# Kernel optimization log

Hardware: AMD Instinct MI355X
Metric: run time of the kernel (lower is better)

## Reference

```python
import jax, jax.numpy as jnp
import numpy as np

N0, N1, N2, N3, B = 120000, 20000, 6000, 1600, 64
E1, E2, E3 = 480000, 144000, 38400
KS = 5  # kernel size per dim; K = 125 total


def spline_basis(pseudo, ks=KS):
    # open B-spline basis, degree 1, over [0,1]^3 (torch_spline_conv semantics)
    p = pseudo * (ks - 1)                       # (E,3)
    lo = jnp.clip(jnp.floor(p), 0.0, ks - 2.0)  # (E,3)
    f = p - lo                                  # fractional part
    bits = jnp.array([[(s >> d) & 1 for d in range(3)] for s in range(8)],
                     dtype=jnp.float32)         # (8,3) corner offsets
    w = jnp.where(bits[None] > 0, f[:, None, :], 1.0 - f[:, None, :])  # (E,8,3)
    basis = w[..., 0] * w[..., 1] * w[..., 2]   # (E,8)
    strides = jnp.array([1.0, ks, ks * ks], dtype=jnp.float32)
    kidx = ((lo[:, None, :] + bits[None]) * strides).sum(-1).astype(jnp.int32)  # (E,8)
    return basis, kidx


def spline_conv(x, edge_index, pseudo, W, root, bias, num_nodes):
    src, dst = edge_index[0], edge_index[1]
    basis, kidx = spline_basis(pseudo)                   # (E,8), (E,8)
    XW = jnp.einsum('ni,kio->nko', x, W)                 # (N,K,out)
    taps = XW[src[:, None], kidx]                        # (E,8,out) gather
    msg = (taps * basis[..., None]).sum(axis=1)          # (E,out)
    agg = jax.ops.segment_sum(msg, dst, num_segments=num_nodes)
    deg = jax.ops.segment_sum(jnp.ones_like(dst, jnp.float32), dst,
                              num_segments=num_nodes)
    agg = agg / jnp.maximum(deg, 1.0)[:, None]           # mean aggregation
    return agg + x @ root + bias


def seg_max(x, seg, n):
    v = jax.ops.segment_max(x, seg, num_segments=n)
    return jnp.where(jnp.isfinite(v), v, 0.0)  # empty voxels -> 0


def setup_inputs() -> dict:
    key = jax.random.key(0)
    ks = jax.random.split(key, 24)
    return {
        'x0': jax.random.uniform(ks[0], (N0, 1), jnp.float32),
        'cluster0': jax.random.randint(ks[1], (N0,), 0, N1),
        'edge1': jax.random.randint(ks[2], (2, E1), 0, N1),
        'pseudo1': jax.random.uniform(ks[3], (E1, 3), jnp.float32),
        'W1': jax.random.normal(ks[4], (125, 1, 64), jnp.float32) * 0.1,
        'root1': jax.random.normal(ks[5], (1, 64), jnp.float32) * 0.1,
        'b1': jnp.zeros((64,), jnp.float32),
        'cluster1': jax.random.randint(ks[6], (N1,), 0, N2),
        'edge2': jax.random.randint(ks[7], (2, E2), 0, N2),
        'pseudo2': jax.random.uniform(ks[8], (E2, 3), jnp.float32),
        'W2': jax.random.normal(ks[9], (125, 64, 64), jnp.float32) * 0.05,
        'root2': jax.random.normal(ks[10], (64, 64), jnp.float32) * 0.05,
        'b2': jnp.zeros((64,), jnp.float32),
        'cluster2': jax.random.randint(ks[11], (N2,), 0, N3),
        'edge3': jax.random.randint(ks[12], (2, E3), 0, N3),
        'pseudo3': jax.random.uniform(ks[13], (E3, 3), jnp.float32),
        'W3': jax.random.normal(ks[14], (125, 64, 128), jnp.float32) * 0.05,
        'root3': jax.random.normal(ks[15], (64, 128), jnp.float32) * 0.05,
        'b3': jnp.zeros((128,), jnp.float32),
        'cluster3': jax.random.randint(ks[16], (N3,), 0, B * 8),
        'fc1_w': jax.random.normal(ks[17], (1024, 256), jnp.float32) * 0.03,
        'fc1_b': jnp.zeros((256,), jnp.float32),
        'fc2_w': jax.random.normal(ks[18], (256, 10), jnp.float32) * 0.06,
        'fc2_b': jnp.zeros((10,), jnp.float32),
    }


def reference(x0, cluster0, edge1, pseudo1, W1, root1, b1,
              cluster1, edge2, pseudo2, W2, root2, b2,
              cluster2, edge3, pseudo3, W3, root3, b3,
              cluster3, fc1_w, fc1_b, fc2_w, fc2_b):
    x = seg_max(x0, cluster0, N1)                       # sparse voxel max pool 1
    x = jax.nn.elu(spline_conv(x, edge1, pseudo1, W1, root1, b1, N1))
    x = seg_max(x, cluster1, N2)                        # pool 2
    x = jax.nn.elu(spline_conv(x, edge2, pseudo2, W2, root2, b2, N2))
    x = seg_max(x, cluster2, N3)                        # pool 3
    x = jax.nn.elu(spline_conv(x, edge3, pseudo3, W3, root3, b3, N3))
    x = seg_max(x, cluster3, B * 8)                     # dense 2x2x2 voxel pool
    x = x.reshape(B, 8 * 128)
    x = jax.nn.elu(x @ fc1_w + fc1_b)
    x = x @ fc2_w + fc2_b
    return jax.nn.log_softmax(x, axis=1)
```

## Files before the change

kernel.cpp:

```cpp
#include <hip/hip_runtime.h>
#include <hip/hip_bf16.h>
#include <hip/hip_fp16.h>
#include <math.h>

#define N0c 120000
#define N1c 20000
#define N2c 6000
#define N3c 1600
#define E1c 480000
#define E2c 144000
#define E3c 38400

#define HB1 256
#define HB2 480
#define HB3 160
#define WCVB 125
#define WC1B 32
#define SS0B  469
#define OFFB  345
#define DECB  79

typedef __attribute__((ext_vector_type(8))) short short8;
typedef __attribute__((ext_vector_type(8))) _Float16 half8;
typedef __attribute__((ext_vector_type(4))) float f32x4;

__device__ __forceinline__ float eluf(float x) {
    return x > 0.0f ? x : expm1f(x);
}

__device__ __forceinline__ unsigned f2sort(float f) {
    unsigned u = __float_as_uint(f);
    return (u & 0x80000000u) ? ~u : (u | 0x80000000u);
}
__device__ __forceinline__ float sort2f(unsigned u) {
    unsigned bits = (u & 0x80000000u) ? (u & 0x7FFFFFFFu) : ~u;
    return __uint_as_float(bits);
}
__device__ __forceinline__ unsigned short f2bf(float v) {
    unsigned u = __float_as_uint(v);
    unsigned r = (u + 0x7FFFu + ((u >> 16) & 1u)) >> 16;
    return (unsigned short)r;
}
__device__ __forceinline__ unsigned short f2h(float v) {
    return __half_as_ushort(__float2half(v));
}
__device__ __forceinline__ float h2f(unsigned short u) {
    return __half2float(__ushort_as_half(u));
}

__global__ __launch_bounds__(256) void hist_all(
    const int* __restrict__ edge1, const int* __restrict__ edge2,
    const int* __restrict__ edge3,
    const float* __restrict__ pseudo2, const float* __restrict__ pseudo3,
    const float* __restrict__ W2, const float* __restrict__ W3,
    const float* __restrict__ W1,
    const float* __restrict__ x0, const int* __restrict__ cluster0,
    int* __restrict__ blockCnt1, int* __restrict__ binTot1,
    int* __restrict__ blockCnt2, int* __restrict__ binTot2, int* __restrict__ cntD2,
    int* __restrict__ blockCnt3, int* __restrict__ binTot3, int* __restrict__ cntD3,
    unsigned short* __restrict__ W2t, unsigned short* __restrict__ W3t,
    unsigned short* __restrict__ W1t,
    unsigned* __restrict__ xm1)
{
    __shared__ float smf[64 * 129];
    int* h = (int*)smf;
    int b = blockIdx.x, t = threadIdx.x;
    if (b < HB1) {
        for (int i = t; i < 1250; i += 256) h[i] = 0;
        __syncthreads();
        for (int e = b * 256 + t; e < E1c; e += HB1 * 256)
            atomicAdd(&h[edge1[E1c + e] >> 4], 1);
        __syncthreads();
        for (int i = t; i < 1250; i += 256) {
            int v = h[i];
            blockCnt1[i * HB1 + b] = v;
            if (v) atomicAdd(&binTot1[i], v);
        }
    } else if (b < HB1 + HB2 + HB3) {
        bool is2 = b < HB1 + HB2;
        int rb = is2 ? (b - HB1) : (b - HB1 - HB2);
        int nblk = is2 ? HB2 : HB3;
        int E = is2 ? E2c : E3c;
        const int* edge = is2 ? edge2 : edge3;
        const float* pseudo = is2 ? pseudo2 : pseudo3;
        int* blockCnt = is2 ? blockCnt2 : blockCnt3;
        int* binTot = is2 ? binTot2 : binTot3;
        int* dstCnt = is2 ? cntD2 : cntD3;
        int nb = is2 ? HB2 : HB3;
        if (t < 64) h[t] = 0;
        __syncthreads();
        for (int e = rb * 256 + t; e < E; e += nblk * 256) {
            int c = 0, mul = 1;
            #pragma unroll
            for (int d = 0; d < 3; d++) {
                float p = pseudo[e * 3 + d] * 4.0f;
                float l = fminf(fmaxf(floorf(p), 0.0f), 3.0f);
                c += (int)l * mul;
                mul <<= 2;
            }
            atomicAdd(&h[c], 1);
            atomicAdd(&dstCnt[edge[E + e]], 1);
        }
        __syncthreads();
        if (t < 64) {
            int v = h[t];
            blockCnt[t * nb + rb] = v;
            if (v) atomicAdd(&binTot[t], v);
        }
    } else if (b < HB1 + HB2 + HB3 + WCVB) {
        int k = b - (HB1 + HB2 + HB3);
        for (int idx = t; idx < 4096; idx += 256) {
            int n = idx & 63, ic = idx >> 6;
            smf[ic * 65 + n] = W2[((size_t)k * 64 + ic) * 64 + n];
        }
        __syncthreads();
        for (int idx = t; idx < 4096; idx += 256) {
            int ic = idx & 63, n = idx >> 6;
            int f = ic >> 5, q = (ic >> 3) & 3, hh = ic & 7;
            int cb = n >> 4, mc = n & 15;
            W2t[((size_t)((k * 2 + f) * 4 + cb)) * 512 + mc * 32 + q * 8 + hh]
                = f2bf(smf[ic * 65 + n]);
        }
    } else if (b < HB1 + HB2 + HB3 + 2 * WCVB) {
        int k = b - (HB1 + HB2 + HB3 + WCVB);
        for (int idx = t; idx < 8192; idx += 256) {
            int n = idx & 127, ic = idx >> 7;
            smf[ic * 129 + n] = W3[((size_t)k * 64 + ic) * 128 + n];
        }
        __syncthreads();
        for (int idx = t; idx < 8192; idx += 256) {
            int ic = idx & 63, n = idx >> 6;
            int f = ic >> 5, q = (ic >> 3) & 3, hh = ic & 7;
            int cb = n >> 4, mc = n & 15;
            W3t[((size_t)((k * 2 + f) * 8 + cb)) * 512 + mc * 32 + q * 8 + hh]
                = f2bf(smf[ic * 129 + n]);
        }
    } else if (b < HB1 + HB2 + HB3 + 2 * WCVB + WC1B) {
        int idx = (b - (HB1 + HB2 + HB3 + 2 * WCVB)) * 256 + t;
        int n = idx >> 7, k = idx & 127;
        W1t[idx] = (k < 125) ? f2h(W1[k * 64 + n]) : (unsigned short)0;
    } else {
        int idx = (b - (HB1 + HB2 + HB3 + 2 * WCVB + WC1B)) * 256 + t;
        if (idx < N0c)
            atomicMax(&xm1[cluster0[idx]], f2sort(x0[idx]));
    }
}

__global__ __launch_bounds__(256) void plan_tot(
    const int* __restrict__ binTot1, int* __restrict__ start1,
    const int* __restrict__ binTot2, int* __restrict__ binCnt2,
    int* __restrict__ binStart2, int* __restrict__ blkPrefix2,
    int* __restrict__ chunkBin2, int* __restrict__ chunkOff2,
    const int* __restrict__ binTot3, int* __restrict__ binCnt3,
    int* __restrict__ binStart3, int* __restrict__ blkPrefix3,
    int* __restrict__ chunkBin3, int* __restrict__ chunkOff3,
    const int* __restrict__ cntD2, int* __restrict__ dstStart2,
    const int* __restrict__ cntD3, int* __restrict__ dstStart3)
{
    __shared__ int ps[256];
    __shared__ int ps64[64];
    int t = threadIdx.x;

    {
        int loc[5];
        int s = 0;
        #pragma unroll
        for (int i = 0; i < 5; i++) {
            int bin = t * 5 + i;
            int v = (bin < 1250) ? binTot1[bin] : 0;
            loc[i] = v;
            s += v;
        }
        ps[t] = s;
        __syncthreads();
        for (int ofs = 1; ofs < 256; ofs <<= 1) {
            int add = (t >= ofs) ? ps[t - ofs] : 0;
            __syncthreads();
            ps[t] += add;
            __syncthreads();
        }
        int run = (t == 0) ? 0 : ps[t - 1];
        #pragma unroll
        for (int i = 0; i < 5; i++) {
            int bin = t * 5 + i;
            if (bin < 1250) {
                start1[bin] = run;
                run += loc[i];
            }
        }
        if (t == 255) start1[1250] = run;
    }
    __syncthreads();

    if (t < 64) {
        int v = binTot2[t];
        binCnt2[t] = v;
        ps64[t] = v;
    }
    __syncthreads();
    if (t == 0) {
        int s2 = 0, p = 0;
        for (int c = 0; c < 64; c++) {
            int v = ps64[c];
            binStart2[c] = s2;
            blkPrefix2[c] = p;
            s2 += v;
            p += (v + 63) >> 6;
        }
        binStart2[64] = s2;
        blkPrefix2[64] = p;
    }
    __syncthreads();
    if (t < 64) {
        int nch = (binCnt2[t] + 63) >> 6;
        int base = blkPrefix2[t];
        for (int j = 0; j < nch; j++) {
            chunkBin2[base + j] = t;
            chunkOff2[base + j] = j;
        }
    }
    __syncthreads();

    if (t < 64) {
        int v = binTot3[t];
        binCnt3[t] = v;
        ps64[t] = v;
    }
    __syncthreads();
    if (t == 0) {
        int s3 = 0, p = 0;
        for (int c = 0; c < 64; c++) {
            int v = ps64[c];
            binStart3[c] = s3;
            blkPrefix3[c] = p;
            s3 += v;
            p += (v + 63) >> 6;
        }
        binStart3[64] = s3;
        blkPrefix3[64] = p;
    }
    __syncthreads();
    if (t < 64) {
        int nch = (binCnt3[t] + 63) >> 6;
        int base = blkPrefix3[t];
        for (int j = 0; j < nch; j++) {
            chunkBin3[base + j] = t;
            chunkOff3[base + j] = j;
        }
    }
    __syncthreads();

    {
        int locd[24];
        int sd = 0;
        #pragma unroll
        for (int i = 0; i < 24; i++) {
            int bin = t * 24 + i;
            int vv = (bin < N2c) ? cntD2[bin] : 0;
            locd[i] = vv;
            sd += vv;
        }
        ps[t] = sd;
        __syncthreads();
        for (int ofs = 1; ofs < 256; ofs <<= 1) {
            int add = (t >= ofs) ? ps[t - ofs] : 0;
            __syncthreads();
            ps[t] += add;
            __syncthreads();
        }
        int rund = (t == 0) ? 0 : ps[t - 1];
        #pragma unroll
        for (int i = 0; i < 24; i++) {
            int bin = t * 24 + i;
            if (bin < N2c) { dstStart2[bin] = rund; rund += locd[i]; }
        }
        if (t == 255) dstStart2[N2c] = ps[255];
    }
    __syncthreads();

    {
        int locd[7];
        int sd = 0;
        #pragma unroll
        for (int i = 0; i < 7; i++) {
            int bin = t * 7 + i;
            int vv = (bin < N3c) ? cntD3[bin] : 0;
            locd[i] = vv;
            sd += vv;
        }
        ps[t] = sd;
        __syncthreads();
        for (int ofs = 1; ofs < 256; ofs <<= 1) {
            int add = (t >= ofs) ? ps[t - ofs] : 0;
            __syncthreads();
            ps[t] += add;
            __syncthreads();
        }
        int rund = (t == 0) ? 0 : ps[t - 1];
        #pragma unroll
        for (int i = 0; i < 7; i++) {
            int bin = t * 7 + i;
            if (bin < N3c) { dstStart3[bin] = rund; rund += locd[i]; }
        }
        if (t == 255) dstStart3[N3c] = ps[255];
    }
}

__global__ __launch_bounds__(256) void off_all(
    const int* __restrict__ blockCnt1, const int* __restrict__ start1,
    int* __restrict__ blockOff1,
    const int* __restrict__ blockCnt2, const int* __restrict__ binStart2,
    int* __restrict__ blockOff2,
    const int* __restrict__ blockCnt3, const int* __restrict__ binStart3,
    int* __restrict__ blockOff3,
    unsigned* __restrict__ xm1)
{
    if (blockIdx.x >= OFFB) {
        int idx = (blockIdx.x - OFFB) * 256 + threadIdx.x;
        if (idx < N1c) {
            float f = sort2f(xm1[idx]);
            unsigned bb = __float_as_uint(f);
            if ((bb & 0x7F800000u) == 0x7F800000u) f = 0.0f;
            ((float*)xm1)[idx] = f;
        }
        return;
    }
    int wid = (blockIdx.x * 256 + threadIdx.x) >> 6;
    int lane = threadIdx.x & 63;
    if (wid >= 1250 + 64 + 64) return;
    const int* c;
    int* o;
    int run, width;
    if (wid < 1250) {
        c = blockCnt1 + (size_t)wid * HB1;
        o = blockOff1 + (size_t)wid * HB1;
        run = start1[wid];
        width = HB1;
    } else if (wid < 1250 + 64) {
        int bin = wid - 1250;
        c = blockCnt2 + (size_t)bin * HB2;
        o = blockOff2 + (size_t)bin * HB2;
        run = binStart2[bin];
        width = HB2;
    } else {
        int bin = wid - 1314;
        c = blockCnt3 + (size_t)bin * HB3;
        o = blockOff3 + (size_t)bin * HB3;
        run = binStart3[bin];
        width = HB3;
    }
    for (int base = 0; base < width; base += 64) {
        int b = base + lane;
        int v = (b < width) ? c[b] : 0;
        int inc = v;
        #pragma unroll
        for (int ofs = 1; ofs < 64; ofs <<= 1) {
            int u = __shfl_up(inc, ofs);
            if (lane >= ofs) inc += u;
        }
        if (b < width) o[b] = run + inc - v;
        run += __shfl(inc, 63);
    }
}

__global__ __launch_bounds__(256) void scatter_all(
    const int* __restrict__ edge1, const float* __restrict__ pseudo1,
    const int* __restrict__ edge2, const float* __restrict__ pseudo2,
    const int* __restrict__ edge3, const float* __restrict__ pseudo3,
    const int* __restrict__ blockOff1,
    const int* __restrict__ blockOff2, const int* __restrict__ blockOff3,
    int4* __restrict__ rec1, int4* __restrict__ rec2, int4* __restrict__ rec3,
    const float* __restrict__ x1,
    const int* __restrict__ dstStart2, const int* __restrict__ dstStart3,
    int* __restrict__ curD2, int* __restrict__ curD3,
    int* __restrict__ posList2, int* __restrict__ posList3)
{
    __shared__ int cur[1250];
    int b = blockIdx.x, t = threadIdx.x;
    if (b < HB1) {
        for (int i = t; i < 1250; i += 256) cur[i] = blockOff1[(size_t)i * HB1 + b];
        __syncthreads();
        for (int e = b * 256 + t; e < E1c; e += HB1 * 256) {
            int src = edge1[e], dst = edge1[E1c + e];
            float f[3];
            int kbase = 0, mul5 = 1;
            #pragma unroll
            for (int d = 0; d < 3; d++) {
                float pp = pseudo1[e * 3 + d] * 4.0f;
                float l = fminf(fmaxf(floorf(pp), 0.0f), 3.0f);
                f[d] = pp - l;
                kbase += (int)l * mul5;
                mul5 *= 5;
            }
            float xv = x1[src];
            int p = atomicAdd(&cur[dst >> 4], 1);
            rec1[p] = make_int4(((int)f2h(f[0]) << 16) | (kbase << 4) | (dst & 15),
                                __float_as_int(xv), __float_as_int(f[1]),
                                __float_as_int(f[2]));
        }
    } else {
        bool is2 = b < HB1 + HB2;
        int rb = is2 ? (b - HB1) : (b - HB1 - HB2);
        int nblk = is2 ? HB2 : HB3;
        int E = is2 ? E2c : E3c;
        const int* edge = is2 ? edge2 : edge3;
        const float* pseudo = is2 ? pseudo2 : pseudo3;
        const int* blockOff = is2 ? blockOff2 : blockOff3;
        int4* rec = is2 ? rec2 : rec3;
        const int* dstStart = is2 ? dstStart2 : dstStart3;
        int* curD = is2 ? curD2 : curD3;
        int* posList = is2 ? posList2 : posList3;
        int nb = is2 ? HB2 : HB3;
        if (t < 64) cur[t] = blockOff[(size_t)t * nb + rb];
        __syncthreads();
        for (int e = rb * 256 + t; e < E; e += nblk * 256) {
            int src = edge[e], dst = edge[E + e];
            float f[3];
            int c = 0, mul = 1;
            #pragma unroll
            for (int d = 0; d < 3; d++) {
                float pp = pseudo[e * 3 + d] * 4.0f;
                float l = fminf(fmaxf(floorf(pp), 0.0f), 3.0f);
                f[d] = pp - l;
                c += (int)l * mul;
                mul <<= 2;
            }
            int p = atomicAdd(&cur[c], 1);
            rec[p] = make_int4(src | (dst << 16),
                               __float_as_int(f[0]), __float_as_int(f[1]),
                               __float_as_int(f[2]));
            int qd = dstStart[dst] + atomicAdd(&curD[dst], 1);
            posList[qd] = p;
        }
    }
}

__global__ __launch_bounds__(256) void conv1_block(
    const int4* __restrict__ rec, const float* __restrict__ x,
    const int* __restrict__ start,
    const unsigned short* __restrict__ W1t,
    const float* __restrict__ root,
    const float* __restrict__ bias, const int* __restrict__ cl,
    unsigned* __restrict__ xmOut) {
    __shared__ float T[16][128];
    __shared__ unsigned short T16[16][136];
    __shared__ int degL[16];
    int b = blockIdx.x;
    int t = threadIdx.x;
    for (int j = t; j < 2048; j += 256) ((float*)T)[j] = 0.0f;
    if (t < 16) degL[t] = 0;
    __syncthreads();
    int s0 = start[b], s1 = start[b + 1];
    for (int i = s0 + t; i < s1; i += 256) {
        int4 r = rec[i];
        int ln = r.x & 15;
        int kbase = (r.x >> 4) & 127;
        float f0 = h2f((unsigned short)((unsigned)r.x >> 16));
        float xv = __int_as_float(r.y);
        float f1 = __int_as_float(r.z);
        float f2 = __int_as_float(r.w);
        #pragma unroll
        for (int s = 0; s < 8; s++) {
            int b0 = s & 1, b1 = (s >> 1) & 1, b2 = (s >> 2) & 1;
            float w0 = b0 ? f0 : 1.0f - f0;
            float w1 = b1 ? f1 : 1.0f - f1;
            float w2 = b2 ? f2 : 1.0f - f2;
            int k = kbase + b0 + 5 * b1 + 25 * b2;
            atomicAdd(&T[ln][k], xv * w0 * w1 * w2);
        }
        atomicAdd(&degL[ln], 1);
    }
    __syncthreads();
    for (int j = t; j < 2048; j += 256) {
        int node = j >> 7, k = j & 127;
        T16[node][k] = f2h(T[node][k]);
    }
    __syncthreads();
    int w = t >> 6, lane = t & 63;
    int q = lane >> 4, mcol = lane & 15;
    const unsigned short* ar = &T16[mcol][0];
    half8 a0 = *(const half8*)(ar + q * 8);
    half8 a1 = *(const half8*)(ar + 32 + q * 8);
    half8 a2 = *(const half8*)(ar + 64 + q * 8);
    half8 a3 = *(const half8*)(ar + 96 + q * 8);
    int ch = w * 16 + mcol;
    const unsigned short* br = W1t + (size_t)ch * 128;
    half8 b0 = *(const half8*)(br + q * 8);
    half8 b1 = *(const half8*)(br + 32 + q * 8);
    half8 b2 = *(const half8*)(br + 64 + q * 8);
    half8 b3 = *(const half8*)(br + 96 + q * 8);
    f32x4 c = (f32x4){0.0f, 0.0f, 0.0f, 0.0f};
    c = __builtin_amdgcn_mfma_f32_16x16x32_f16(a0, b0, c, 0, 0, 0);
    c = __builtin_amdgcn_mfma_f32_16x16x32_f16(a1, b1, c, 0, 0, 0);
    c = __builtin_amdgcn_mfma_f32_16x16x32_f16(a2, b2, c, 0, 0, 0);
    c = __builtin_amdgcn_mfma_f32_16x16x32_f16(a3, b3, c, 0, 0, 0);
    int v0 = b << 4;
    float rt_ = root[ch], bi = bias[ch];
    #pragma unroll
    for (int r = 0; r < 4; r++) {
        int node = q * 4 + r;
        int v = v0 + node;
        float d = fmaxf((float)degL[node], 1.0f);
        float val = eluf(c[r] / d + x[v] * rt_ + bi);
        atomicMax(&xmOut[((size_t)cl[v] << 6) + ch], f2sort(val));
    }
}

__global__ void decode_cvt(unsigned* __restrict__ buf,
                           unsigned short* __restrict__ xb, int total) {
    int idx = blockIdx.x * blockDim.x + threadIdx.x;
    if (idx >= total) return;
    float f = sort2f(buf[idx]);
    unsigned b = __float_as_uint(f);
    if ((b & 0x7F800000u) == 0x7F800000u) f = 0.0f;
    ((float*)buf)[idx] = f;
    xb[idx] = f2bf(f);
}

template<int COUT>
__global__ __launch_bounds__(256) void spline_mfma(
    const int4* __restrict__ recs,
    const unsigned short* __restrict__ Wt,
    const unsigned short* __restrict__ xb,
    const int* __restrict__ binStart,
    const int* __restrict__ binCnt,
    const int* __restrict__ blkPrefix,
    const int* __restrict__ chunkBin,
    const int* __restrict__ chunkOff,
    unsigned short* __restrict__ msg)
{
    __shared__ float basisS[4][8][64];
    __shared__ int srcS[4][64];

    int w = threadIdx.x >> 6, lane = threadIdx.x & 63;
    int c = blockIdx.x * 4 + w;
    if (c >= blkPrefix[64]) return;
    int bin = chunkBin[c];
    int chunk = chunkOff[c];
    int cnt = binCnt[bin];

    {
        int pos = chunk * 64 + lane;
        bool act = pos < cnt;
        int4 r = act ? recs[binStart[bin] + pos] : make_int4(0, 0, 0, 0);
        srcS[w][lane] = r.x & 0xFFFF;
        float f0 = __int_as_float(r.y);
        float f1 = __int_as_float(r.z);
        float f2 = __int_as_float(r.w);
        #pragma unroll
        for (int s = 0; s < 8; s++) {
            float w0 = (s & 1) ? f0 : 1.0f - f0;
            float w1 = (s & 2) ? f1 : 1.0f - f1;
            float w2 = (s & 4) ? f2 : 1.0f - f2;
            basisS[w][s][lane] = act ? (w0 * w1 * w2) : 0.0f;
        }
    }
    __builtin_amdgcn_wave_barrier();
    __threadfence_block();

    int lo0 = bin & 3, lo1 = (bin >> 2) & 3, lo2 = bin >> 4;
    int kbase = lo0 + 5 * lo1 + 25 * lo2;
    int colOff = blockIdx.y << 5;
    int q = lane >> 4;
    int mcol = lane & 15;
    int cb0 = colOff >> 4;
    int lof = (mcol << 5) + (q << 3);

    short8 afr[4][2];
    #pragma unroll
    for (int rt = 0; rt < 4; rt++) {
        int src = srcS[w][rt * 16 + mcol];
        const unsigned short* xr = xb + ((size_t)src << 6) + q * 8;
        afr[rt][0] = *(const short8*)(xr);
        afr[rt][1] = *(const short8*)(xr + 32);
    }

    f32x4 acc[4][2];
    #pragma unroll
    for (int rt = 0; rt < 4; rt++)
        #pragma unroll
        for (int nt = 0; nt < 2; nt++)
            acc[rt][nt] = (f32x4){0.0f, 0.0f, 0.0f, 0.0f};
    const f32x4 zero4 = {0.0f, 0.0f, 0.0f, 0.0f};

    short8 bcur[2][2];
    {
        #pragma unroll
        for (int nt = 0; nt < 2; nt++) {
            bcur[nt][0] = *(const short8*)(Wt + ((size_t)((kbase * 2 + 0) * (COUT >> 4) + cb0 + nt)) * 512 + lof);
            bcur[nt][1] = *(const short8*)(Wt + ((size_t)((kbase * 2 + 1) * (COUT >> 4) + cb0 + nt)) * 512 + lof);
        }
    }
    #pragma unroll 1
    for (int s = 0; s < 8; s++) {
        short8 bnx[2][2];
        if (s < 7) {
            int sn = s + 1;
            int kn = kbase + (sn & 1) + 5 * ((sn >> 1) & 1) + 25 * (sn >> 2);
            #pragma unroll
            for (int nt = 0; nt < 2; nt++) {
                bnx[nt][0] = *(const short8*)(Wt + ((size_t)((kn * 2 + 0) * (COUT >> 4) + cb0 + nt)) * 512 + lof);
                bnx[nt][1] = *(const short8*)(Wt + ((size_t)((kn * 2 + 1) * (COUT >> 4) + cb0 + nt)) * 512 + lof);
            }
        }
        #pragma unroll
        for (int rt = 0; rt < 4; rt++) {
            f32x4 ct[2];
            #pragma unroll
            for (int nt = 0; nt < 2; nt++) {
                ct[nt] = __builtin_amdgcn_mfma_f32_16x16x32_bf16(afr[rt][0], bcur[nt][0], zero4, 0, 0, 0);
                ct[nt] = __builtin_amdgcn_mfma_f32_16x16x32_bf16(afr[rt][1], bcur[nt][1], ct[nt], 0, 0, 0);
            }
            #pragma unroll
            for (int r = 0; r < 4; r++) {
                float bs = basisS[w][s][rt * 16 + q * 4 + r];
                #pragma unroll
                for (int nt = 0; nt < 2; nt++)
                    acc[rt][nt][r] = fmaf(bs, ct[nt][r], acc[rt][nt][r]);
            }
        }
        if (s < 7) {
            #pragma unroll
            for (int nt = 0; nt < 2; nt++) {
                bcur[nt][0] = bnx[nt][0];
                bcur[nt][1] = bnx[nt][1];
            }
        }
    }

    int base = binStart[bin] + chunk * 64;
    #pragma unroll
    for (int rt = 0; rt < 4; rt++) {
        #pragma unroll
        for (int r = 0; r < 4; r++) {
            int row = rt * 16 + q * 4 + r;
            if (chunk * 64 + row < cnt) {
                unsigned short* mp = msg + (size_t)(base + row) * COUT + colOff + mcol;
                mp[0]  = f2h(acc[rt][0][r]);
                mp[16] = f2h(acc[rt][1][r]);
            }
        }
    }
}

__global__ __launch_bounds__(256) void agg_update64(
    const unsigned short* __restrict__ msg, const int* __restrict__ posList,
    const int* __restrict__ dstStart,
    const float* __restrict__ xm, const float* __restrict__ root,
    const float* __restrict__ bias, const int* __restrict__ cl,
    unsigned* __restrict__ xmOut, int nNodes) {
    __shared__ float xsh[4][64];
    int w = threadIdx.x >> 6, lane = threadIdx.x & 63;
    int v = blockIdx.x * 4 + w;
    if (v >= nNodes) return;
    xsh[w][lane] = xm[((size_t)v << 6) + lane];
    int s0 = dstStart[v], s1 = dstStart[v + 1];
    float a0 = 0.0f, a1 = 0.0f, a2 = 0.0f, a3 = 0.0f;
    int i = s0;
    for (; i + 4 <= s1; i += 4) {
        int p0 = posList[i], p1 = posList[i + 1];
        int p2 = posList[i + 2], p3 = posList[i + 3];
        a0 += h2f(msg[((size_t)p0 << 6) + lane]);
        a1 += h2f(msg[((size_t)p1 << 6) + lane]);
        a2 += h2f(msg[((size_t)p2 << 6) + lane]);
        a3 += h2f(msg[((size_t)p3 << 6) + lane]);
    }
    for (; i < s1; i++)
        a0 += h2f(msg[((size_t)posList[i] << 6) + lane]);
    float a = (a0 + a1 + a2 + a3) / fmaxf((float)(s1 - s0), 1.0f);
    float r = 0.0f;
    #pragma unroll 8
    for (int j = 0; j < 64; j++)
        r = fmaf(xsh[w][j], root[(j << 6) + lane], r);
    float val = eluf(a + r + bias[lane]);
    atomicMax(&xmOut[((size_t)cl[v] << 6) + lane], f2sort(val));
}

__global__ __launch_bounds__(256) void agg_update128(
    const unsigned short* __restrict__ msg, const int* __restrict__ posList,
    const int* __restrict__ dstStart,
    const float* __restrict__ xm, const float* __restrict__ root,
    const float* __restrict__ bias, const int* __restrict__ cl,
    unsigned* __restrict__ xmOut, int nNodes) {
    __shared__ float xsh[4][64];
    int w = threadIdx.x >> 6, lane = threadIdx.x & 63;
    int v = blockIdx.x * 4 + w;
    if (v >= nNodes) return;
    xsh[w][lane] = xm[((size_t)v << 6) + lane];
    int s0 = dstStart[v], s1 = dstStart[v + 1];
    float c0a = 0.0f, c0b = 0.0f, c1a = 0.0f, c1b = 0.0f;
    int i = s0;
    for (; i + 2 <= s1; i += 2) {
        int p0 = posList[i], p1 = posList[i + 1];
        const unsigned short* m0 = msg + ((size_t)p0 << 7);
        const unsigned short* m1 = msg + ((size_t)p1 << 7);
        c0a += h2f(m0[lane]); c0b += h2f(m0[64 + lane]);
        c1a += h2f(m1[lane]); c1b += h2f(m1[64 + lane]);
    }
    for (; i < s1; i++) {
        const unsigned short* m0 = msg + ((size_t)posList[i] << 7);
        c0a += h2f(m0[lane]); c0b += h2f(m0[64 + lane]);
    }
    float dinv = 1.0f / fmaxf((float)(s1 - s0), 1.0f);
    float aa0 = (c0a + c1a) * dinv;
    float aa1 = (c0b + c1b) * dinv;
    float r0 = 0.0f, r1 = 0.0f;
    #pragma unroll 8
    for (int j = 0; j < 64; j++) {
        float xi = xsh[w][j];
        r0 = fmaf(xi, root[(j << 7) + lane], r0);
        r1 = fmaf(xi, root[(j << 7) + 64 + lane], r1);
    }
    unsigned* orow = xmOut + ((size_t)cl[v] << 7);
    atomicMax(&orow[lane], f2sort(eluf(aa0 + r0 + bias[lane])));
    atomicMax(&orow[64 + lane], f2sort(eluf(aa1 + r1 + bias[lane + 64])));
}

__global__ __launch_bounds__(256) void fc1_split(
    const unsigned* __restrict__ xin, const float* __restrict__ w1,
    float* __restrict__ h) {
    __shared__ float xsh[128];
    int row = blockIdx.x, ks = blockIdx.y;
    int o = threadIdx.x;
    if (o < 128) {
        float f = sort2f(xin[row * 1024 + ks * 128 + o]);
        unsigned bb = __float_as_uint(f);
        if ((bb & 0x7F800000u) == 0x7F800000u) f = 0.0f;
        xsh[o] = f;
    }
    __syncthreads();
    float acc = 0.0f;
    const float* wp = w1 + (size_t)ks * 128 * 256 + o;
    #pragma unroll 8
    for (int i = 0; i < 128; i++)
        acc = fmaf(xsh[i], wp[i * 256], acc);
    atomicAdd(&h[row * 256 + o], acc);
}

__global__ __launch_bounds__(64) void fc2_k(
    const float* __restrict__ h, const float* __restrict__ b1,
    const float* __restrict__ w2, const float* __restrict__ b2,
    float* __restrict__ out) {
    __shared__ float hs[256];
    __shared__ float lg[10];
    int row = blockIdx.x;
    int t = threadIdx.x;
    for (int i = t; i < 256; i += 64) hs[i] = eluf(h[row * 256 + i] + b1[i]);
    __syncthreads();
    if (t < 10) {
        float a = b2[t];
        for (int i = 0; i < 256; i++) a = fmaf(hs[i], w2[i * 10 + t], a);
        lg[t] = a;
    }
    __syncthreads();
    if (t < 10) {
        float m = -1e30f;
        #pragma unroll
        for (int j = 0; j < 10; j++) m = fmaxf(m, lg[j]);
        float sum = 0.0f;
        #pragma unroll
        for (int j = 0; j < 10; j++) sum += expf(lg[j] - m);
        out[row * 10 + t] = lg[t] - m - logf(sum);
    }
}

extern "C" void kernel_launch(void* const* d_in, const int* in_sizes, int n_in,
                              void* d_out, int out_size, void* d_ws, size_t ws_size,
                              hipStream_t stream) {
    const float* x0      = (const float*)d_in[0];
    const int*   cluster0= (const int*)d_in[1];
    const int*   edge1   = (const int*)d_in[2];
    const float* pseudo1 = (const float*)d_in[3];
    const float* W1      = (const float*)d_in[4];
    const float* root1   = (const float*)d_in[5];
    const float* b1      = (const float*)d_in[6];
    const int*   cluster1= (const int*)d_in[7];
    const int*   edge2   = (const int*)d_in[8];
    const float* pseudo2 = (const float*)d_in[9];
    const float* W2      = (const float*)d_in[10];
    const float* root2   = (const float*)d_in[11];
    const float* b2      = (const float*)d_in[12];
    const int*   cluster2= (const int*)d_in[13];
    const int*   edge3   = (const int*)d_in[14];
    const float* pseudo3 = (const float*)d_in[15];
    const float* W3      = (const float*)d_in[16];
    const float* root3   = (const float*)d_in[17];
    const float* b3      = (const float*)d_in[18];
    const int*   cluster3= (const int*)d_in[19];
    const float* fc1_w   = (const float*)d_in[20];
    const float* fc1_b   = (const float*)d_in[21];
    const float* fc2_w   = (const float*)d_in[22];
    const float* fc2_b   = (const float*)d_in[23];
    float* out = (float*)d_out;

    float* ws = (float*)d_ws;
    size_t off = 0;
    float* xm1  = ws + off; off += 20480;
    float* xm2  = ws + off; off += (size_t)N2c * 64;
    float* xm3  = ws + off; off += (size_t)N3c * 64;
    float* xm4  = ws + off; off += 512 * 128;
    float* h1   = ws + off; off += 64 * 256;
    int* cntD2   = (int*)(ws + off); off += 6016;
    int* cntD3   = (int*)(ws + off); off += 1664;
    int* curD2   = (int*)(ws + off); off += 6016;
    int* curD3   = (int*)(ws + off); off += 1664;
    int* binTot1 = (int*)(ws + off); off += 1280;
    int* binTot2 = (int*)(ws + off); off += 64;
    int* binTot3 = (int*)(ws + off); off += 64;
    size_t zeroFloats = off;
    int4* rec1 = (int4*)(ws + off); off += (size_t)E1c * 4;
    int4* rec2 = (int4*)(ws + off); off += (size_t)E2c * 4;
    int4* rec3 = (int4*)(ws + off); off += (size_t)E3c * 4;
    unsigned short* W2t = (unsigned short*)(ws + off); off += 256000;
    unsigned short* W3t = (unsigned short*)(ws + off); off += 512000;
    unsigned short* W1t = (unsigned short*)(ws + off); off += 4096;
    unsigned short* xb2 = (unsigned short*)(ws + off); off += 192000;
    unsigned short* xb3 = (unsigned short*)(ws + off); off += 51200;
    int* start1    = (int*)(ws + off); off += 1280;
    int* blockCnt1 = (int*)(ws + off); off += (size_t)HB1 * 1250;
    int* blockOff1 = (int*)(ws + off); off += (size_t)HB1 * 1250;
    int* blockCnt2 = (int*)(ws + off); off += (size_t)HB2 * 64;
    int* blockOff2 = (int*)(ws + off); off += (size_t)HB2 * 64;
    int* blockCnt3 = (int*)(ws + off); off += (size_t)HB3 * 64;
    int* blockOff3 = (int*)(ws + off); off += (size_t)HB3 * 64;
    int* binCnt2   = (int*)(ws + off); off += 64;
    int* binStart2 = (int*)(ws + off); off += 80;
    int* blkPrefix2= (int*)(ws + off); off += 80;
    int* chunkBin2 = (int*)(ws + off); off += 2560;
    int* chunkOff2 = (int*)(ws + off); off += 2560;
    int* binCnt3   = (int*)(ws + off); off += 64;
    int* binStart3 = (int*)(ws + off); off += 80;
    int* blkPrefix3= (int*)(ws + off); off += 80;
    int* chunkBin3 = (int*)(ws + off); off += 768;
    int* chunkOff3 = (int*)(ws + off); off += 768;
    int* dstStart2 = (int*)(ws + off); off += 6016;
    int* dstStart3 = (int*)(ws + off); off += 1664;
    int* posList2  = (int*)(ws + off); off += E2c;
    int* posList3  = (int*)(ws + off); off += E3c;
    unsigned short* msg = (unsigned short*)(ws + off); off += (size_t)E2c * 32;

    hipMemsetAsync(d_ws, 0, zeroFloats * sizeof(float), stream);

    hist_all<<<HB1 + HB2 + HB3 + 2 * WCVB + WC1B + SS0B, 256, 0, stream>>>(
        edge1, edge2, edge3, pseudo2, pseudo3, W2, W3, W1, x0, cluster0,
        blockCnt1, binTot1, blockCnt2, binTot2, cntD2,
        blockCnt3, binTot3, cntD3, W2t, W3t, W1t, (unsigned*)xm1);

    plan_tot<<<1, 256, 0, stream>>>(
        binTot1, start1,
        binTot2, binCnt2, binStart2, blkPrefix2, chunkBin2, chunkOff2,
        binTot3, binCnt3, binStart3, blkPrefix3, chunkBin3, chunkOff3,
        cntD2, dstStart2, cntD3, dstStart3);

    off_all<<<OFFB + DECB, 256, 0, stream>>>(
        blockCnt1, start1, blockOff1,
        blockCnt2, binStart2, blockOff2,
        blockCnt3, binStart3, blockOff3, (unsigned*)xm1);

    scatter_all<<<HB1 + HB2 + HB3, 256, 0, stream>>>(
        edge1, pseudo1, edge2, pseudo2, edge3, pseudo3,
        blockOff1, blockOff2, blockOff3, rec1, rec2, rec3, xm1,
        dstStart2, dstStart3, curD2, curD3, posList2, posList3);

    conv1_block<<<1250, 256, 0, stream>>>(rec1, xm1, start1, W1t, root1, b1,
                                          cluster1, (unsigned*)xm2);
    decode_cvt<<<(N2c * 64) / 256, 256, 0, stream>>>((unsigned*)xm2, xb2, N2c * 64);

    spline_mfma<64><<<dim3((E2c / 64 + 64 + 3) / 4, 2), 256, 0, stream>>>(
        rec2, W2t, xb2, binStart2, binCnt2, blkPrefix2, chunkBin2, chunkOff2, msg);
    agg_update64<<<(N2c + 3) / 4, 256, 0, stream>>>(msg, posList2, dstStart2,
                                                    xm2, root2, b2, cluster2,
                                                    (unsigned*)xm3, N2c);
    decode_cvt<<<(N3c * 64) / 256, 256, 0, stream>>>((unsigned*)xm3, xb3, N3c * 64);

    spline_mfma<128><<<dim3((E3c / 64 + 64 + 3) / 4, 4), 256, 0, stream>>>(
        rec3, W3t, xb3, binStart3, binCnt3, blkPrefix3, chunkBin3, chunkOff3, msg);
    agg_update128<<<(N3c + 3) / 4, 256, 0, stream>>>(msg, posList3, dstStart3,
                                                     xm3, root3, b3, cluster3,
                                                     (unsigned*)xm4, N3c);

    fc1_split<<<dim3(64, 8), 256, 0, stream>>>((unsigned*)xm4, fc1_w, h1);
    fc2_k<<<64, 64, 0, stream>>>(h1, fc1_b, fc2_w, fc2_b, out);
}
```

Measured before the change: 294.8 us.

## Store spline messages in column-split planes via LDS-staged vector writes

The MFMA spline kernel now stages each 16-row accumulator tile in shared memory and writes each message row as 16-byte vector stores. Output goes into a per-blockIdx.y plane layout (32 columns per plane) instead of interleaved rows of COUT. The aggregation kernels read from the matching planes. The aim is to replace scattered 2-byte global stores with coalesced wide stores, at the cost of extra LDS traffic and wave barriers per tile.

Result: no change. 298.1 us (+1.1%).

```diff
diff --git a/kernel.cpp b/kernel.cpp
--- a/kernel.cpp
+++ b/kernel.cpp
@@ -527,10 +527,11 @@
     const int* __restrict__ blkPrefix,
     const int* __restrict__ chunkBin,
     const int* __restrict__ chunkOff,
-    unsigned short* __restrict__ msg)
+    unsigned short* __restrict__ msg, int eTot)
 {
     __shared__ float basisS[4][8][64];
     __shared__ int srcS[4][64];
+    __shared__ unsigned short CtS[4][16][40];
 
     int w = threadIdx.x >> 6, lane = threadIdx.x & 63;
     int c = blockIdx.x * 4 + w;
@@ -629,17 +630,26 @@
     }
 
     int base = binStart[bin] + chunk * 64;
+    unsigned short* msgP = msg + (size_t)blockIdx.y * eTot * 32;
+    int lrow = lane >> 2, seg = lane & 3;
     #pragma unroll
     for (int rt = 0; rt < 4; rt++) {
         #pragma unroll
         for (int r = 0; r < 4; r++) {
-            int row = rt * 16 + q * 4 + r;
-            if (chunk * 64 + row < cnt) {
-                unsigned short* mp = msg + (size_t)(base + row) * COUT + colOff + mcol;
-                mp[0]  = f2h(acc[rt][0][r]);
-                mp[16] = f2h(acc[rt][1][r]);
-            }
-        }
+            int row = q * 4 + r;
+            #pragma unroll
+            for (int nt = 0; nt < 2; nt++)
+                CtS[w][row][nt * 16 + mcol] = f2h(acc[rt][nt][r]);
+        }
+        __builtin_amdgcn_wave_barrier();
+        __threadfence_block();
+        int grow = rt * 16 + lrow;
+        if (chunk * 64 + grow < cnt) {
+            short8 vv = *(const short8*)&CtS[w][lrow][seg * 8];
+            *(short8*)(msgP + (((size_t)(base + grow)) << 5) + seg * 8) = vv;
+        }
+        __builtin_amdgcn_wave_barrier();
+        __threadfence_block();
     }
 }
 
@@ -654,19 +664,21 @@
     int v = blockIdx.x * 4 + w;
     if (v >= nNodes) return;
     xsh[w][lane] = xm[((size_t)v << 6) + lane];
+    const unsigned short* mpl = msg + ((size_t)(lane >> 5)) * ((size_t)E2c * 32);
+    int cl32 = lane & 31;
     int s0 = dstStart[v], s1 = dstStart[v + 1];
     float a0 = 0.0f, a1 = 0.0f, a2 = 0.0f, a3 = 0.0f;
     int i = s0;
     for (; i + 4 <= s1; i += 4) {
         int p0 = posList[i], p1 = posList[i + 1];
         int p2 = posList[i + 2], p3 = posList[i + 3];
-        a0 += h2f(msg[((size_t)p0 << 6) + lane]);
-        a1 += h2f(msg[((size_t)p1 << 6) + lane]);
-        a2 += h2f(msg[((size_t)p2 << 6) + lane]);
-        a3 += h2f(msg[((size_t)p3 << 6) + lane]);
+        a0 += h2f(mpl[((size_t)p0 << 5) + cl32]);
+        a1 += h2f(mpl[((size_t)p1 << 5) + cl32]);
+        a2 += h2f(mpl[((size_t)p2 << 5) + cl32]);
+        a3 += h2f(mpl[((size_t)p3 << 5) + cl32]);
     }
     for (; i < s1; i++)
-        a0 += h2f(msg[((size_t)posList[i] << 6) + lane]);
+        a0 += h2f(mpl[((size_t)posList[i] << 5) + cl32]);
     float a = (a0 + a1 + a2 + a3) / fmaxf((float)(s1 - s0), 1.0f);
     float r = 0.0f;
     #pragma unroll 8
@@ -687,19 +699,20 @@
     int v = blockIdx.x * 4 + w;
     if (v >= nNodes) return;
     xsh[w][lane] = xm[((size_t)v << 6) + lane];
+    const unsigned short* mA = msg + ((size_t)(lane >> 5)) * ((size_t)E3c * 32);
+    const unsigned short* mB = msg + ((size_t)(2 + (lane >> 5))) * ((size_t)E3c * 32);
+    int cl32 = lane & 31;
     int s0 = dstStart[v], s1 = dstStart[v + 1];
     float c0a = 0.0f, c0b = 0.0f, c1a = 0.0f, c1b = 0.0f;
     int i = s0;
     for (; i + 2 <= s1; i += 2) {
         int p0 = posList[i], p1 = posList[i + 1];
-        const unsigned short* m0 = msg + ((size_t)p0 << 7);
-        const unsigned short* m1 = msg + ((size_t)p1 << 7);
-        c0a += h2f(m0[lane]); c0b += h2f(m0[64 + lane]);
-        c1a += h2f(m1[lane]); c1b += h2f(m1[64 + lane]);
+        c0a += h2f(mA[((size_t)p0 << 5) + cl32]); c0b += h2f(mB[((size_t)p0 << 5) + cl32]);
+        c1a += h2f(mA[((size_t)p1 << 5) + cl32]); c1b += h2f(mB[((size_t)p1 << 5) + cl32]);
     }
     for (; i < s1; i++) {
-        const unsigned short* m0 = msg + ((size_t)posList[i] << 7);
-        c0a += h2f(m0[lane]); c0b += h2f(m0[64 + lane]);
+        int p0 = posList[i];
+        c0a += h2f(mA[((size_t)p0 << 5) + cl32]); c0b += h2f(mB[((size_t)p0 << 5) + cl32]);
     }
     float dinv = 1.0f / fmaxf((float)(s1 - s0), 1.0f);
     float aa0 = (c0a + c1a) * dinv;
@@ -867,14 +880,16 @@
     decode_cvt<<<(N2c * 64) / 256, 256, 0, stream>>>((unsigned*)xm2, xb2, N2c * 64);
 
     spline_mfma<64><<<dim3((E2c / 64 + 64 + 3) / 4, 2), 256, 0, stream>>>(
-        rec2, W2t, xb2, binStart2, binCnt2, blkPrefix2, chunkBin2, chunkOff2, msg);
+        rec2, W2t, xb2, binStart2, binCnt2, blkPrefix2, chunkBin2, chunkOff2,
+        msg, E2c);
     agg_update64<<<(N2c + 3) / 4, 256, 0, stream>>>(msg, posList2, dstStart2,
                                                     xm2, root2, b2, cluster2,
                                                     (unsigned*)xm3, N2c);
     decode_cvt<<<(N3c * 64) / 256, 256, 0, stream>>>((unsigned*)xm3, xb3, N3c * 64);
 
     spline_mfma<128><<<dim3((E3c / 64 + 64 + 3) / 4, 4), 256, 0, stream>>>(
-        rec3, W3t, xb3, binStart3, binCnt3, blkPrefix3, chunkBin3, chunkOff3, msg);
+        rec3, W3t, xb3, binStart3, binCnt3, blkPrefix3, chunkBin3, chunkOff3,
+        msg, E3c);
     agg_update128<<<(N3c + 3) / 4, 256, 0, stream>>>(msg, posList3, dstStart3,
                                                      xm3, root3, b3, cluster3,
                                                      (unsigned*)xm4, N3c);
```
